# Kernel optimization log

Hardware: AMD Instinct MI355X
Metric: run time of the kernel (lower is better)

Reference implementation:

```python
import jax, jax.numpy as jnp
import numpy as np

TOP_K = 6
ROUTED_SCALE = 2.5

def setup_inputs() -> dict:
    key = jax.random.key(0)
    ks = jax.random.split(key, 8)
    T, H, I, E = 1024, 2048, 1024, 16
    Is = 2 * I  # shared expert intermediate = n_shared_experts * moe_intermediate_size
    s = 0.02
    return {
        "hidden_states": jax.random.normal(ks[0], (T, H), jnp.float32),
        "gate_w": jax.random.normal(ks[1], (E, H), jnp.float32) * s,          # ReplicatedLinear [out,in]
        "e_score_correction_bias": jax.random.normal(ks[2], (E,), jnp.float32) * s,
        "w1": jax.random.normal(ks[3], (E, 2 * I, H), jnp.float32) * s,       # merged gate_up per expert
        "w2": jax.random.normal(ks[4], (E, H, I), jnp.float32) * s,           # down proj per expert
        "shared_w1": jax.random.normal(ks[5], (2 * Is, H), jnp.float32) * s,  # shared gate_up
        "shared_w2": jax.random.normal(ks[6], (H, Is), jnp.float32) * s,      # shared down
    }

def _silu_and_mul(gu):
    g, u = jnp.split(gu, 2, axis=-1)
    return jax.nn.silu(g) * u

def _moe_forward(hidden_states, gate_w, e_score_correction_bias, w1, w2, shared_w1, shared_w2):
    T, H = hidden_states.shape
    E = gate_w.shape[0]
    # shared expert path (Dots1MLP)
    shared_out = _silu_and_mul(hidden_states @ shared_w1.T) @ shared_w2.T  # [T,H]
    # gating in fp32 (moe_gating_fp32=True)
    router_logits = hidden_states.astype(jnp.float32) @ gate_w.astype(jnp.float32).T  # [T,E]
    # noaux_tc routing: sigmoid scores + correction bias for selection, raw sigmoid for weights
    scores = jax.nn.sigmoid(router_logits)
    choice = scores + e_score_correction_bias[None, :]
    _, topk_idx = jax.lax.top_k(choice, TOP_K)                              # [T,k]
    topk_w = jnp.take_along_axis(scores, topk_idx, axis=1)                  # [T,k]
    topk_w = topk_w / jnp.sum(topk_w, axis=-1, keepdims=True)
    topk_w = topk_w * ROUTED_SCALE
    # dense combine weights [T,E] (top-k slots per token, rest zero)
    route_w = jnp.zeros((T, E), jnp.float32)
    route_w = route_w.at[jnp.arange(T)[:, None], topk_idx].set(topk_w)
    # expert MLPs (computed for all experts, masked by routing weights)
    gu = jnp.einsum('th,egh->teg', hidden_states, w1)                       # [T,E,2I]
    h = _silu_and_mul(gu)                                                   # [T,E,I]
    routed_out = jnp.einsum('tei,ehi,te->th', h, w2, route_w.astype(hidden_states.dtype))
    return routed_out + shared_out                                          # [T,H]

def reference(hidden_states, gate_w, e_score_correction_bias, w1, w2, shared_w1, shared_w2):
    return _moe_forward(hidden_states, gate_w, e_score_correction_bias, w1, w2, shared_w1, shared_w2)
```

## Files before the change

kernel.cpp:

```cpp
#include <hip/hip_runtime.h>
#include <hip/hip_bf16.h>

#define T_TOK 1024
#define NEXP 16
#define HD 2048
#define TOPK 6

typedef __attribute__((ext_vector_type(8))) short short8;
typedef __attribute__((ext_vector_type(4))) float floatx4;

__device__ __forceinline__ short f2bf(float f) {
    unsigned u = __builtin_bit_cast(unsigned, f);
    u += 0x7FFFu + ((u >> 16) & 1u);
    return (short)(u >> 16);
}

typedef __attribute__((address_space(1))) void gvoid;
typedef __attribute__((address_space(3))) void lvoid;
__device__ __forceinline__ void gload_lds16(const void* g, void* l) {
    __builtin_amdgcn_global_load_lds((gvoid*)g, (lvoid*)l, 16, 0, 0);
}

__global__ __launch_bounds__(256) void cvt_all(
    const float* __restrict__ X, const float* __restrict__ W1,
    const float* __restrict__ W2, const float* __restrict__ SW1,
    const float* __restrict__ SW2,
    short* __restrict__ Xb, short* __restrict__ W1b, short* __restrict__ W2b,
    short* __restrict__ SW1b, short* __restrict__ SW2b)
{
    const int C0 = 524288;
    const int C1 = C0 + 16777216;
    const int C2 = C1 + 8388608;
    const int C3 = C2 + 2097152;
    const int C4 = C3 + 1048576;
    for (int i = blockIdx.x * blockDim.x + threadIdx.x; i < C4;
         i += gridDim.x * blockDim.x) {
        const float* s; short* d; int l;
        if (i < C0)      { s = X;   d = Xb;   l = i; }
        else if (i < C1) { s = W1;  d = W1b;  l = i - C0; }
        else if (i < C2) { s = W2;  d = W2b;  l = i - C1; }
        else if (i < C3) { s = SW1; d = SW1b; l = i - C2; }
        else             { s = SW2; d = SW2b; l = i - C3; }
        const float4 v = ((const float4*)s)[l];
        short4 o;
        o.x = f2bf(v.x); o.y = f2bf(v.y); o.z = f2bf(v.z); o.w = f2bf(v.w);
        ((short4*)d)[l] = o;
    }
}

__global__ __launch_bounds__(64) void router_kernel(
    const float* __restrict__ X, const float* __restrict__ GW,
    const float* __restrict__ bias, int* __restrict__ counts,
    int* __restrict__ lists, int* __restrict__ tok_e,
    int* __restrict__ tok_pos, float* __restrict__ tok_w)
{
    const int t = blockIdx.x;
    const int l = threadIdx.x;
    const float* x = X + (size_t)t * HD;
    float acc[NEXP];
#pragma unroll
    for (int e = 0; e < NEXP; ++e) acc[e] = 0.f;
    for (int k = l; k < HD; k += 64) {
        const float xv = x[k];
#pragma unroll
        for (int e = 0; e < NEXP; ++e) acc[e] += xv * GW[e * HD + k];
    }
#pragma unroll
    for (int e = 0; e < NEXP; ++e) {
        float v = acc[e];
#pragma unroll
        for (int m = 32; m >= 1; m >>= 1) v += __shfl_xor(v, m, 64);
        acc[e] = v;
    }
    if (l == 0) {
        float s[NEXP], choice[NEXP];
#pragma unroll
        for (int e = 0; e < NEXP; ++e) {
            s[e] = 1.f / (1.f + __expf(-acc[e]));
            choice[e] = s[e] + bias[e];
        }
        int idx[TOPK]; float wv[TOPK]; float wsum = 0.f;
        bool used[NEXP];
#pragma unroll
        for (int e = 0; e < NEXP; ++e) used[e] = false;
        for (int j = 0; j < TOPK; ++j) {
            float best = -1e30f; int bi = 0;
            for (int e = 0; e < NEXP; ++e)
                if (!used[e] && choice[e] > best) { best = choice[e]; bi = e; }
            used[bi] = true; idx[j] = bi; wv[j] = s[bi]; wsum += s[bi];
        }
        const float scale = 2.5f / wsum;
        for (int j = 0; j < TOPK; ++j) {
            const int e = idx[j];
            const int pos = atomicAdd(&counts[e], 1);
            lists[e * T_TOK + pos] = t;
            tok_e[t * TOPK + j] = e;
            tok_pos[t * TOPK + j] = pos;
            tok_w[t * TOPK + j] = wv[j] * scale;
        }
    }
}

__global__ void offsets_kernel(const int* __restrict__ counts, int* __restrict__ offs)
{
    if (threadIdx.x == 0 && blockIdx.x == 0) {
        int a = 0;
        for (int e = 0; e < NEXP; ++e) { offs[e] = a; a += counts[e]; }
    }
}

__global__ __launch_bounds__(256) void gateup2(
    const short* __restrict__ Xbf, const short* __restrict__ W1bf,
    const short* __restrict__ SW1bf,
    const int* __restrict__ counts, const int* __restrict__ offs,
    const int* __restrict__ lists,
    short* __restrict__ h_r, short* __restrict__ h_s)
{
    __shared__ short sA[2][128][32];
    __shared__ short sB[2][128][32];
    const int z = blockIdx.z;
    const bool shx = (z == NEXP);
    if (!shx && blockIdx.x >= 16) return;
    const int cnt = shx ? T_TOK : counts[z];
    const int m0 = blockIdx.y * 128;
    if (m0 >= cnt) return;
    const int Ih = shx ? 2048 : 1024;
    const int i0 = blockIdx.x * 64;
    const short* W = shx ? SW1bf : (W1bf + (size_t)z * 2048 * HD);
    short* Hout = shx ? h_s : h_r;
    const int hbase = shx ? 0 : offs[z];

    const int tid = threadIdx.x;
    const int wave = tid >> 6, lane = tid & 63;
    const int srow0 = wave * 32 + (lane >> 2);
    const int srow1 = srow0 + 16;
    const int scol = (lane & 3) * 8;

    int ar0 = m0 + srow0; if (ar0 > cnt - 1) ar0 = cnt - 1;
    int ar1 = m0 + srow1; if (ar1 > cnt - 1) ar1 = cnt - 1;
    const int tok0 = shx ? ar0 : lists[z * T_TOK + ar0];
    const int tok1 = shx ? ar1 : lists[z * T_TOK + ar1];
    const short* ag0 = Xbf + (size_t)tok0 * HD + scol;
    const short* ag1 = Xbf + (size_t)tok1 * HD + scol;
    const int br0 = (srow0 < 64) ? (i0 + srow0) : (Ih + i0 + srow0 - 64);
    const int br1 = (srow1 < 64) ? (i0 + srow1) : (Ih + i0 + srow1 - 64);
    const short* bg0 = W + (size_t)br0 * HD + scol;
    const short* bg1 = W + (size_t)br1 * HD + scol;

    const int wx = wave & 1, wy = wave >> 1;
    const int l15 = lane & 15, l4 = lane >> 4;

    floatx4 acc[4][4];
#pragma unroll
    for (int a = 0; a < 4; ++a)
#pragma unroll
        for (int b = 0; b < 4; ++b) acc[a][b] = (floatx4){0.f, 0.f, 0.f, 0.f};

    gload_lds16(ag0, &sA[0][wave * 32][0]);
    gload_lds16(ag1, &sA[0][wave * 32 + 16][0]);
    gload_lds16(bg0, &sB[0][wave * 32][0]);
    gload_lds16(bg1, &sB[0][wave * 32 + 16][0]);

    for (int k0 = 0; k0 < HD; k0 += 32) {
        const int p = (k0 >> 5) & 1;
        __syncthreads();
        if (k0 + 32 < HD) {
            const int q = p ^ 1;
            gload_lds16(ag0 + k0 + 32, &sA[q][wave * 32][0]);
            gload_lds16(ag1 + k0 + 32, &sA[q][wave * 32 + 16][0]);
            gload_lds16(bg0 + k0 + 32, &sB[q][wave * 32][0]);
            gload_lds16(bg1 + k0 + 32, &sB[q][wave * 32 + 16][0]);
        }
        short8 af[4], bfr[4];
#pragma unroll
        for (int mc = 0; mc < 4; ++mc)
            af[mc] = *(const short8*)&sA[p][wy * 64 + mc * 16 + l15][l4 * 8];
#pragma unroll
        for (int cb = 0; cb < 4; ++cb) {
            const int br = ((cb < 2) ? 0 : 64) + wx * 32 + (cb & 1) * 16 + l15;
            bfr[cb] = *(const short8*)&sB[p][br][l4 * 8];
        }
#pragma unroll
        for (int mc = 0; mc < 4; ++mc)
#pragma unroll
            for (int cb = 0; cb < 4; ++cb)
                acc[mc][cb] = __builtin_amdgcn_mfma_f32_16x16x32_bf16(
                    af[mc], bfr[cb], acc[mc][cb], 0, 0, 0);
    }

#pragma unroll
    for (int mc = 0; mc < 4; ++mc)
#pragma unroll
        for (int cb = 0; cb < 2; ++cb)
#pragma unroll
            for (int r = 0; r < 4; ++r) {
                const int mrel = wy * 64 + mc * 16 + l4 * 4 + r;
                if (m0 + mrel < cnt) {
                    const float g = acc[mc][cb][r];
                    const float u = acc[mc][cb + 2][r];
                    const float h = g / (1.f + __expf(-g)) * u;
                    const int col = i0 + wx * 32 + cb * 16 + l15;
                    Hout[(size_t)(hbase + m0 + mrel) * Ih + col] = f2bf(h);
                }
            }
}

__global__ __launch_bounds__(256) void down2(
    const short* __restrict__ h_r, const short* __restrict__ h_s,
    const short* __restrict__ W2bf, const short* __restrict__ SW2bf,
    const int* __restrict__ counts, const int* __restrict__ offs,
    float* __restrict__ h2, float* __restrict__ sh_out)
{
    __shared__ short sA[2][128][32];
    __shared__ short sB[2][128][32];
    const int z = blockIdx.z;
    const bool shx = (z == NEXP);
    const int cnt = shx ? T_TOK : counts[z];
    const int m0 = blockIdx.y * 128;
    if (m0 >= cnt) return;
    const int Kih = shx ? 2048 : 1024;
    const int n0 = blockIdx.x * 128;
    const short* A = shx ? h_s : h_r;
    const short* W = shx ? SW2bf : (W2bf + (size_t)z * HD * 1024);
    float* outb = shx ? sh_out : h2;
    const int hbase = shx ? 0 : offs[z];

    const int tid = threadIdx.x;
    const int wave = tid >> 6, lane = tid & 63;
    const int srow0 = wave * 32 + (lane >> 2);
    const int srow1 = srow0 + 16;
    const int scol = (lane & 3) * 8;

    int ar0 = m0 + srow0; if (ar0 > cnt - 1) ar0 = cnt - 1;
    int ar1 = m0 + srow1; if (ar1 > cnt - 1) ar1 = cnt - 1;
    const short* ag0 = A + (size_t)(hbase + ar0) * Kih + scol;
    const short* ag1 = A + (size_t)(hbase + ar1) * Kih + scol;
    const short* bg0 = W + (size_t)(n0 + srow0) * Kih + scol;
    const short* bg1 = W + (size_t)(n0 + srow1) * Kih + scol;

    const int wx = wave & 1, wy = wave >> 1;
    const int l15 = lane & 15, l4 = lane >> 4;

    floatx4 acc[4][4];
#pragma unroll
    for (int a = 0; a < 4; ++a)
#pragma unroll
        for (int b = 0; b < 4; ++b) acc[a][b] = (floatx4){0.f, 0.f, 0.f, 0.f};

    gload_lds16(ag0, &sA[0][wave * 32][0]);
    gload_lds16(ag1, &sA[0][wave * 32 + 16][0]);
    gload_lds16(bg0, &sB[0][wave * 32][0]);
    gload_lds16(bg1, &sB[0][wave * 32 + 16][0]);

    for (int k0 = 0; k0 < Kih; k0 += 32) {
        const int p = (k0 >> 5) & 1;
        __syncthreads();
        if (k0 + 32 < Kih) {
            const int q = p ^ 1;
            gload_lds16(ag0 + k0 + 32, &sA[q][wave * 32][0]);
            gload_lds16(ag1 + k0 + 32, &sA[q][wave * 32 + 16][0]);
            gload_lds16(bg0 + k0 + 32, &sB[q][wave * 32][0]);
            gload_lds16(bg1 + k0 + 32, &sB[q][wave * 32 + 16][0]);
        }
        short8 af[4], bfr[4];
#pragma unroll
        for (int mc = 0; mc < 4; ++mc)
            af[mc] = *(const short8*)&sA[p][wy * 64 + mc * 16 + l15][l4 * 8];
#pragma unroll
        for (int cb = 0; cb < 4; ++cb)
            bfr[cb] = *(const short8*)&sB[p][wx * 64 + cb * 16 + l15][l4 * 8];
#pragma unroll
        for (int mc = 0; mc < 4; ++mc)
#pragma unroll
            for (int cb = 0; cb < 4; ++cb)
                acc[mc][cb] = __builtin_amdgcn_mfma_f32_16x16x32_bf16(
                    af[mc], bfr[cb], acc[mc][cb], 0, 0, 0);
    }

#pragma unroll
    for (int mc = 0; mc < 4; ++mc)
#pragma unroll
        for (int r = 0; r < 4; ++r) {
            const int mrel = wy * 64 + mc * 16 + l4 * 4 + r;
            if (m0 + mrel >= cnt) continue;
            float* orow = outb + (size_t)(hbase + m0 + mrel) * HD + n0 + wx * 64 + l15;
#pragma unroll
            for (int cb = 0; cb < 4; ++cb)
                orow[cb * 16] = acc[mc][cb][r];
        }
}

__global__ __launch_bounds__(256) void combine_kernel(
    const float* __restrict__ h2, const float* __restrict__ sh_out,
    const int* __restrict__ offs, const int* __restrict__ tok_e,
    const int* __restrict__ tok_pos, const float* __restrict__ tok_w,
    float* __restrict__ out)
{
    const int t = blockIdx.x;
    int rows[TOPK]; float w[TOPK];
#pragma unroll
    for (int j = 0; j < TOPK; ++j) {
        const int e = tok_e[t * TOPK + j];
        rows[j] = offs[e] + tok_pos[t * TOPK + j];
        w[j] = tok_w[t * TOPK + j];
    }
    for (int c = threadIdx.x * 4; c < HD; c += 256 * 4) {
        float4 acc = *(const float4*)(sh_out + (size_t)t * HD + c);
#pragma unroll
        for (int j = 0; j < TOPK; ++j) {
            const float4 v = *(const float4*)(h2 + (size_t)rows[j] * HD + c);
            acc.x += w[j] * v.x; acc.y += w[j] * v.y;
            acc.z += w[j] * v.z; acc.w += w[j] * v.w;
        }
        *(float4*)(out + (size_t)t * HD + c) = acc;
    }
}

extern "C" void kernel_launch(void* const* d_in, const int* in_sizes, int n_in,
                              void* d_out, int out_size, void* d_ws, size_t ws_size,
                              hipStream_t stream) {
    const float* X    = (const float*)d_in[0];
    const float* GW   = (const float*)d_in[1];
    const float* BIAS = (const float*)d_in[2];
    const float* W1   = (const float*)d_in[3];
    const float* W2   = (const float*)d_in[4];
    const float* SW1  = (const float*)d_in[5];
    const float* SW2  = (const float*)d_in[6];
    float* out = (float*)d_out;

    char* ws = (char*)d_ws;
    int*   counts  = (int*)(ws + 0);
    int*   offs    = (int*)(ws + 64);
    int*   lists   = (int*)(ws + 256);
    int*   tok_e   = (int*)(ws + 65792);
    int*   tok_pos = (int*)(ws + 90368);
    float* tok_w   = (float*)(ws + 114944);
    short* h_r     = (short*)(ws + 262144);
    short* h_s     = (short*)(ws + 12845056);
    float* h2      = (float*)(ws + 17039360);
    float* sh_out  = (float*)(ws + 67371008);
    short* Xbf     = (short*)(ws + 75759616);
    short* W1bf    = (short*)(ws + 79953920);
    short* W2bf    = (short*)(ws + 214171648);
    short* SW1bf   = (short*)(ws + 281280512);
    short* SW2bf   = (short*)(ws + 298057728);
    const size_t WS_NEEDED = 306446336;
    if (ws_size < WS_NEEDED) return;

    hipMemsetAsync(counts, 0, 64, stream);
    router_kernel<<<T_TOK, 64, 0, stream>>>(X, GW, BIAS, counts, lists,
                                            tok_e, tok_pos, tok_w);
    offsets_kernel<<<1, 64, 0, stream>>>(counts, offs);
    cvt_all<<<4096, 256, 0, stream>>>(X, W1, W2, SW1, SW2,
                                      Xbf, W1bf, W2bf, SW1bf, SW2bf);

    gateup2<<<dim3(32, 8, NEXP + 1), 256, 0, stream>>>(
        Xbf, W1bf, SW1bf, counts, offs, lists, h_r, h_s);

    down2<<<dim3(16, 8, NEXP + 1), 256, 0, stream>>>(
        h_r, h_s, W2bf, SW2bf, counts, offs, h2, sh_out);

    combine_kernel<<<T_TOK, 256, 0, stream>>>(
        h2, sh_out, offs, tok_e, tok_pos, tok_w, out);
}
```

Baseline: 896.0 us.

## Triple-buffer GEMM loads, swizzle LDS, and launch compact tile descriptor grids

Both grouped GEMMs move from a double-buffered loop guarded by full __syncthreads to a three-stage LDS ring. Each step uses a vmcnt-limited waitcnt plus a raw barrier, so two tiles stay in flight. The LDS column index is XOR-swizzled on write and read to cut bank conflicts on the MFMA fragment loads. A descriptor kernel builds compact per-tile work lists so the launch grids drop the many empty blocks of the 3D grid, at the cost of 50% more LDS per block and reliance on hand-coded waitcnt encodings.

```diff
diff --git a/kernel.cpp b/kernel.cpp
--- a/kernel.cpp
+++ b/kernel.cpp
@@ -20,6 +20,9 @@
 __device__ __forceinline__ void gload_lds16(const void* g, void* l) {
     __builtin_amdgcn_global_load_lds((gvoid*)g, (lvoid*)l, 16, 0, 0);
 }
+
+#define WAITCNT_VM4 0x0F74
+#define WAITCNT_VM0 0x0F70
 
 __global__ __launch_bounds__(256) void cvt_all(
     const float* __restrict__ X, const float* __restrict__ W1,
@@ -101,31 +104,56 @@
     }
 }
 
-__global__ void offsets_kernel(const int* __restrict__ counts, int* __restrict__ offs)
-{
-    if (threadIdx.x == 0 && blockIdx.x == 0) {
-        int a = 0;
-        for (int e = 0; e < NEXP; ++e) { offs[e] = a; a += counts[e]; }
-    }
-}
-
-__global__ __launch_bounds__(256) void gateup2(
+__global__ __launch_bounds__(256) void offsets_descs(
+    const int* __restrict__ counts, int* __restrict__ offs,
+    int* __restrict__ gu, int* __restrict__ gu_n,
+    int* __restrict__ dn, int* __restrict__ dn_n)
+{
+    __shared__ int base_gu[NEXP], base_dn[NEXP], nys[NEXP];
+    if (threadIdx.x == 0) {
+        int a = 0, bg = 256, bd = 128;
+        for (int e = 0; e < NEXP; ++e) {
+            offs[e] = a; a += counts[e];
+            const int ny = (counts[e] + 127) >> 7;
+            nys[e] = ny; base_gu[e] = bg; base_dn[e] = bd;
+            bg += ny * 16; bd += ny * 16;
+        }
+        *gu_n = bg; *dn_n = bd;
+    }
+    __syncthreads();
+    for (int i = threadIdx.x; i < 256; i += 256)
+        gu[i] = (NEXP << 16) | ((i >> 5) << 8) | (i & 31);
+    for (int i = threadIdx.x; i < 128; i += 256)
+        dn[i] = (NEXP << 16) | ((i >> 4) << 8) | (i & 15);
+    for (int e = 0; e < NEXP; ++e) {
+        const int nt = nys[e] * 16;
+        for (int i = threadIdx.x; i < nt; i += 256) {
+            const int v = (e << 16) | ((i >> 4) << 8) | (i & 15);
+            gu[base_gu[e] + i] = v;
+            dn[base_dn[e] + i] = v;
+        }
+    }
+}
+
+__global__ __launch_bounds__(256) void gateup3(
     const short* __restrict__ Xbf, const short* __restrict__ W1bf,
     const short* __restrict__ SW1bf,
     const int* __restrict__ counts, const int* __restrict__ offs,
-    const int* __restrict__ lists,
+    const int* __restrict__ lists, const int* __restrict__ descs,
+    const int* __restrict__ ndesc,
     short* __restrict__ h_r, short* __restrict__ h_s)
 {
-    __shared__ short sA[2][128][32];
-    __shared__ short sB[2][128][32];
-    const int z = blockIdx.z;
+    __shared__ short sA[3][128][32];
+    __shared__ short sB[3][128][32];
+    if ((int)blockIdx.x >= *ndesc) return;
+    const int d = descs[blockIdx.x];
+    const int z = d >> 16, yb = (d >> 8) & 255, xb = d & 255;
     const bool shx = (z == NEXP);
-    if (!shx && blockIdx.x >= 16) return;
     const int cnt = shx ? T_TOK : counts[z];
-    const int m0 = blockIdx.y * 128;
+    const int m0 = yb * 128;
     if (m0 >= cnt) return;
     const int Ih = shx ? 2048 : 1024;
-    const int i0 = blockIdx.x * 64;
+    const int i0 = xb * 64;
     const short* W = shx ? SW1bf : (W1bf + (size_t)z * 2048 * HD);
     short* Hout = shx ? h_s : h_r;
     const int hbase = shx ? 0 : offs[z];
@@ -134,7 +162,7 @@
     const int wave = tid >> 6, lane = tid & 63;
     const int srow0 = wave * 32 + (lane >> 2);
     const int srow1 = srow0 + 16;
-    const int scol = (lane & 3) * 8;
+    const int scol = ((lane & 3) ^ ((lane >> 3) & 3)) * 8;
 
     int ar0 = m0 + srow0; if (ar0 > cnt - 1) ar0 = cnt - 1;
     int ar1 = m0 + srow1; if (ar1 > cnt - 1) ar1 = cnt - 1;
@@ -149,6 +177,7 @@
 
     const int wx = wave & 1, wy = wave >> 1;
     const int l15 = lane & 15, l4 = lane >> 4;
+    const int fcol = (l4 ^ ((l15 >> 1) & 3)) * 8;
 
     floatx4 acc[4][4];
 #pragma unroll
@@ -156,29 +185,36 @@
 #pragma unroll
         for (int b = 0; b < 4; ++b) acc[a][b] = (floatx4){0.f, 0.f, 0.f, 0.f};
 
-    gload_lds16(ag0, &sA[0][wave * 32][0]);
-    gload_lds16(ag1, &sA[0][wave * 32 + 16][0]);
-    gload_lds16(bg0, &sB[0][wave * 32][0]);
-    gload_lds16(bg1, &sB[0][wave * 32 + 16][0]);
-
-    for (int k0 = 0; k0 < HD; k0 += 32) {
-        const int p = (k0 >> 5) & 1;
-        __syncthreads();
-        if (k0 + 32 < HD) {
-            const int q = p ^ 1;
-            gload_lds16(ag0 + k0 + 32, &sA[q][wave * 32][0]);
-            gload_lds16(ag1 + k0 + 32, &sA[q][wave * 32 + 16][0]);
-            gload_lds16(bg0 + k0 + 32, &sB[q][wave * 32][0]);
-            gload_lds16(bg1 + k0 + 32, &sB[q][wave * 32 + 16][0]);
+    const int nsteps = HD / 32;
+#pragma unroll
+    for (int pb = 0; pb < 2; ++pb) {
+        const int off = pb * 32;
+        gload_lds16(ag0 + off, &sA[pb][wave * 32][0]);
+        gload_lds16(ag1 + off, &sA[pb][wave * 32 + 16][0]);
+        gload_lds16(bg0 + off, &sB[pb][wave * 32][0]);
+        gload_lds16(bg1 + off, &sB[pb][wave * 32 + 16][0]);
+    }
+
+    int p = 0, q = 2;
+    for (int s = 0; s < nsteps; ++s) {
+        if (s + 1 < nsteps) __builtin_amdgcn_s_waitcnt(WAITCNT_VM4);
+        else                __builtin_amdgcn_s_waitcnt(WAITCNT_VM0);
+        __builtin_amdgcn_s_barrier();
+        if (s + 2 < nsteps) {
+            const int off = (s + 2) * 32;
+            gload_lds16(ag0 + off, &sA[q][wave * 32][0]);
+            gload_lds16(ag1 + off, &sA[q][wave * 32 + 16][0]);
+            gload_lds16(bg0 + off, &sB[q][wave * 32][0]);
+            gload_lds16(bg1 + off, &sB[q][wave * 32 + 16][0]);
         }
         short8 af[4], bfr[4];
 #pragma unroll
         for (int mc = 0; mc < 4; ++mc)
-            af[mc] = *(const short8*)&sA[p][wy * 64 + mc * 16 + l15][l4 * 8];
+            af[mc] = *(const short8*)&sA[p][wy * 64 + mc * 16 + l15][fcol];
 #pragma unroll
         for (int cb = 0; cb < 4; ++cb) {
             const int br = ((cb < 2) ? 0 : 64) + wx * 32 + (cb & 1) * 16 + l15;
-            bfr[cb] = *(const short8*)&sB[p][br][l4 * 8];
+            bfr[cb] = *(const short8*)&sB[p][br][fcol];
         }
 #pragma unroll
         for (int mc = 0; mc < 4; ++mc)
@@ -186,6 +222,8 @@
             for (int cb = 0; cb < 4; ++cb)
                 acc[mc][cb] = __builtin_amdgcn_mfma_f32_16x16x32_bf16(
                     af[mc], bfr[cb], acc[mc][cb], 0, 0, 0);
+        p = (p == 2) ? 0 : p + 1;
+        q = (q == 2) ? 0 : q + 1;
     }
 
 #pragma unroll
@@ -205,21 +243,24 @@
             }
 }
 
-__global__ __launch_bounds__(256) void down2(
+__global__ __launch_bounds__(256) void down3(
     const short* __restrict__ h_r, const short* __restrict__ h_s,
     const short* __restrict__ W2bf, const short* __restrict__ SW2bf,
     const int* __restrict__ counts, const int* __restrict__ offs,
+    const int* __restrict__ descs, const int* __restrict__ ndesc,
     float* __restrict__ h2, float* __restrict__ sh_out)
 {
-    __shared__ short sA[2][128][32];
-    __shared__ short sB[2][128][32];
-    const int z = blockIdx.z;
+    __shared__ short sA[3][128][32];
+    __shared__ short sB[3][128][32];
+    if ((int)blockIdx.x >= *ndesc) return;
+    const int d = descs[blockIdx.x];
+    const int z = d >> 16, yb = (d >> 8) & 255, xb = d & 255;
     const bool shx = (z == NEXP);
     const int cnt = shx ? T_TOK : counts[z];
-    const int m0 = blockIdx.y * 128;
+    const int m0 = yb * 128;
     if (m0 >= cnt) return;
     const int Kih = shx ? 2048 : 1024;
-    const int n0 = blockIdx.x * 128;
+    const int n0 = xb * 128;
     const short* A = shx ? h_s : h_r;
     const short* W = shx ? SW2bf : (W2bf + (size_t)z * HD * 1024);
     float* outb = shx ? sh_out : h2;
@@ -229,7 +270,7 @@
     const int wave = tid >> 6, lane = tid & 63;
     const int srow0 = wave * 32 + (lane >> 2);
     const int srow1 = srow0 + 16;
-    const int scol = (lane & 3) * 8;
+    const int scol = ((lane & 3) ^ ((lane >> 3) & 3)) * 8;
 
     int ar0 = m0 + srow0; if (ar0 > cnt - 1) ar0 = cnt - 1;
     int ar1 = m0 + srow1; if (ar1 > cnt - 1) ar1 = cnt - 1;
@@ -240,6 +281,7 @@
 
     const int wx = wave & 1, wy = wave >> 1;
     const int l15 = lane & 15, l4 = lane >> 4;
+    const int fcol = (l4 ^ ((l15 >> 1) & 3)) * 8;
 
     floatx4 acc[4][4];
 #pragma unroll
@@ -247,34 +289,43 @@
 #pragma unroll
         for (int b = 0; b < 4; ++b) acc[a][b] = (floatx4){0.f, 0.f, 0.f, 0.f};
 
-    gload_lds16(ag0, &sA[0][wave * 32][0]);
-    gload_lds16(ag1, &sA[0][wave * 32 + 16][0]);
-    gload_lds16(bg0, &sB[0][wave * 32][0]);
-    gload_lds16(bg1, &sB[0][wave * 32 + 16][0]);
-
-    for (int k0 = 0; k0 < Kih; k0 += 32) {
-        const int p = (k0 >> 5) & 1;
-        __syncthreads();
-        if (k0 + 32 < Kih) {
-            const int q = p ^ 1;
-            gload_lds16(ag0 + k0 + 32, &sA[q][wave * 32][0]);
-            gload_lds16(ag1 + k0 + 32, &sA[q][wave * 32 + 16][0]);
-            gload_lds16(bg0 + k0 + 32, &sB[q][wave * 32][0]);
-            gload_lds16(bg1 + k0 + 32, &sB[q][wave * 32 + 16][0]);
+    const int nsteps = Kih / 32;
+#pragma unroll
+    for (int pb = 0; pb < 2; ++pb) {
+        const int off = pb * 32;
+        gload_lds16(ag0 + off, &sA[pb][wave * 32][0]);
+        gload_lds16(ag1 + off, &sA[pb][wave * 32 + 16][0]);
+        gload_lds16(bg0 + off, &sB[pb][wave * 32][0]);
+        gload_lds16(bg1 + off, &sB[pb][wave * 32 + 16][0]);
+    }
+
+    int p = 0, q = 2;
+    for (int s = 0; s < nsteps; ++s) {
+        if (s + 1 < nsteps) __builtin_amdgcn_s_waitcnt(WAITCNT_VM4);
+        else                __builtin_amdgcn_s_waitcnt(WAITCNT_VM0);
+        __builtin_amdgcn_s_barrier();
+        if (s + 2 < nsteps) {
+            const int off = (s + 2) * 32;
+            gload_lds16(ag0 + off, &sA[q][wave * 32][0]);
+            gload_lds16(ag1 + off, &sA[q][wave * 32 + 16][0]);
+            gload_lds16(bg0 + off, &sB[q][wave * 32][0]);
+            gload_lds16(bg1 + off, &sB[q][wave * 32 + 16][0]);
         }
         short8 af[4], bfr[4];
 #pragma unroll
         for (int mc = 0; mc < 4; ++mc)
-            af[mc] = *(const short8*)&sA[p][wy * 64 + mc * 16 + l15][l4 * 8];
+            af[mc] = *(const short8*)&sA[p][wy * 64 + mc * 16 + l15][fcol];
 #pragma unroll
         for (int cb = 0; cb < 4; ++cb)
-            bfr[cb] = *(const short8*)&sB[p][wx * 64 + cb * 16 + l15][l4 * 8];
+            bfr[cb] = *(const short8*)&sB[p][wx * 64 + cb * 16 + l15][fcol];
 #pragma unroll
         for (int mc = 0; mc < 4; ++mc)
 #pragma unroll
             for (int cb = 0; cb < 4; ++cb)
                 acc[mc][cb] = __builtin_amdgcn_mfma_f32_16x16x32_bf16(
                     af[mc], bfr[cb], acc[mc][cb], 0, 0, 0);
+        p = (p == 2) ? 0 : p + 1;
+        q = (q == 2) ? 0 : q + 1;
     }
 
 #pragma unroll
@@ -335,6 +386,10 @@
     int*   tok_e   = (int*)(ws + 65792);
     int*   tok_pos = (int*)(ws + 90368);
     float* tok_w   = (float*)(ws + 114944);
+    int*   gu_n    = (int*)(ws + 139776);
+    int*   dn_n    = (int*)(ws + 139780);
+    int*   gu_desc = (int*)(ws + 139840);
+    int*   dn_desc = (int*)(ws + 145024);
     short* h_r     = (short*)(ws + 262144);
     short* h_s     = (short*)(ws + 12845056);
     float* h2      = (float*)(ws + 17039360);
@@ -350,16 +405,15 @@
     hipMemsetAsync(counts, 0, 64, stream);
     router_kernel<<<T_TOK, 64, 0, stream>>>(X, GW, BIAS, counts, lists,
                                             tok_e, tok_pos, tok_w);
-    offsets_kernel<<<1, 64, 0, stream>>>(counts, offs);
+    offsets_descs<<<1, 256, 0, stream>>>(counts, offs, gu_desc, gu_n,
+                                         dn_desc, dn_n);
     cvt_all<<<4096, 256, 0, stream>>>(X, W1, W2, SW1, SW2,
                                       Xbf, W1bf, W2bf, SW1bf, SW2bf);
 
-    gateup2<<<dim3(32, 8, NEXP + 1), 256, 0, stream>>>(
-        Xbf, W1bf, SW1bf, counts, offs, lists, h_r, h_s);
-
-    down2<<<dim3(16, 8, NEXP + 1), 256, 0, stream>>>(
-        h_r, h_s, W2bf, SW2bf, counts, offs, h2, sh_out);
-
+    gateup3<<<1280, 256, 0, stream>>>(Xbf, W1bf, SW1bf, counts, offs, lists,
+                                      gu_desc, gu_n, h_r, h_s);
+    down3<<<1152, 256, 0, stream>>>(h_r, h_s, W2bf, SW2bf, counts, offs,
+                                    dn_desc, dn_n, h2, sh_out);
     combine_kernel<<<T_TOK, 256, 0, stream>>>(
         h2, sh_out, offs, tok_e, tok_pos, tok_w, out);
 }
```

After: 822.6 us. -8.2%, faster.
